# Kernel optimization log

Measured on AMD Instinct MI355X. Metric: run time of the kernel, lower is better.

The kernel has to match this reference:

```python
import jax, jax.numpy as jnp
import numpy as np
import math

DIM, DIM_QK, DIM_V = 1024, 128, 1024
NUM_BUCKETS, MAX_DISTANCE = 32, 128


def silu(x):
    return x * jax.nn.sigmoid(x)


def laplacian_attn_fn(x):
    mu = math.sqrt(0.5)
    std = math.sqrt(0.25 * math.pi)
    return (1.0 + jax.lax.erf((x - mu) / (std * math.sqrt(2.0)))) * 0.5


def rel_pos_bias(seq_len, table, scale):
    # causal T5 bucketing: n = q_pos - k_pos, clamped at 0
    q_pos = jnp.arange(seq_len)
    k_pos = jnp.arange(seq_len)
    rel_pos = k_pos[None, :] - q_pos[:, None]  # [i, j]
    n = jnp.maximum(-rel_pos, 0)
    max_exact = NUM_BUCKETS // 2
    is_small = n < max_exact
    n_safe = jnp.maximum(n, 1).astype(jnp.float32)
    val_if_large = max_exact + (
        jnp.log(n_safe / max_exact) / math.log(MAX_DISTANCE / max_exact)
        * (NUM_BUCKETS - max_exact)
    ).astype(jnp.int32)
    val_if_large = jnp.minimum(val_if_large, NUM_BUCKETS - 1)
    bucket = jnp.where(is_small, n, val_if_large)
    return table[bucket] * scale  # [i, j]


def setup_inputs() -> dict:
    key = jax.random.key(0)
    ks = jax.random.split(key, 8)
    B, S = 4, 2048
    lin_std_qk = 1.0 / math.sqrt(DIM)
    return {
        "x": jax.random.normal(ks[0], (B, S, DIM), dtype=jnp.float32),
        "wqk": jax.random.uniform(ks[1], (DIM, DIM_QK), minval=-lin_std_qk, maxval=lin_std_qk, dtype=jnp.float32),
        "bqk": jnp.zeros((DIM_QK,), dtype=jnp.float32),
        "gamma": 1.0 + 0.02 * jax.random.normal(ks[2], (2, DIM_QK), dtype=jnp.float32),
        "beta": jnp.zeros((2, DIM_QK), dtype=jnp.float32),
        "wv": jax.random.uniform(ks[3], (DIM, DIM_V), minval=-lin_std_qk, maxval=lin_std_qk, dtype=jnp.float32),
        "bv": jnp.zeros((DIM_V,), dtype=jnp.float32),
        "rel_bias": jax.random.normal(ks[4], (NUM_BUCKETS,), dtype=jnp.float32),
    }


def reference(x, wqk, bqk, gamma, beta, wv, bv, rel_bias):
    B, S, _ = x.shape
    qk = silu(x @ wqk + bqk)                       # [B, S, dqk]
    q = qk * gamma[0] + beta[0]
    k = qk * gamma[1] + beta[1]
    v = silu(x @ wv + bv)                          # [B, S, dv]
    scale = 1.0 / S                                # laplacian_attn_fn scaling
    sim = jnp.einsum('bid,bjd->bij', q, k) * scale
    sim = sim + rel_pos_bias(S, rel_bias, DIM_QK ** 0.5)[None, :, :]
    attn = laplacian_attn_fn(sim)
    causal_mask = jnp.triu(jnp.ones((S, S), dtype=bool), k=1)
    attn = jnp.where(causal_mask[None, :, :], 0.0, attn)
    return jnp.einsum('bij,bjd->bid', attn, v)
```

## Files before the change

### kernel.cpp

```cpp
#include <hip/hip_runtime.h>
#include <stdint.h>


#define B_   4
#define S_   2048
#define DIM_ 1024
#define DQK  128
#define DV   1024
#define NQV  1152

typedef __attribute__((ext_vector_type(8))) short short8;
typedef __attribute__((ext_vector_type(4))) float f32x4;

__device__ __forceinline__ uint16_t f32_to_bf16(float f) {
  uint32_t u = __float_as_uint(f);
  u += 0x7FFFu + ((u >> 16) & 1u);
  return (uint16_t)(u >> 16);
}

__device__ __forceinline__ uint32_t pack_bf16(float a, float b) {
  return (uint32_t)f32_to_bf16(a) | ((uint32_t)f32_to_bf16(b) << 16);
}

__device__ __forceinline__ float silu_f(float x) {
  return x * __builtin_amdgcn_rcpf(1.0f + __expf(-x));
}

__device__ __forceinline__ float laplacian_attn(float x) {
  float z  = (x - 0.70710678118654752f) * 0.79788456080286536f;
  float az = fabsf(z);
  float t  = __builtin_amdgcn_rcpf(fmaf(0.3275911f, az, 1.0f));
  float w  = fmaf(1.061405429f, t, -1.453152027f);
  w = fmaf(w, t, 1.421413741f);
  w = fmaf(w, t, -0.284496736f);
  w = fmaf(w, t, 0.254829592f);
  float P  = w * t;
  float E  = __expf(-z * z);
  float ea = fmaf(-P, E, 1.0f);
  float er = copysignf(ea, z);
  return fmaf(0.5f, er, 0.5f);
}

__device__ __forceinline__ void gload16(const uint16_t* g, uint16_t* l) {
  __builtin_amdgcn_global_load_lds(
      (const __attribute__((address_space(1))) void*)g,
      (__attribute__((address_space(3))) void*)l, 16, 0, 0);
}

template <int MT, int NT, int DEPTH>
__device__ __forceinline__ void wave_gemm_t(
    const uint16_t* __restrict__ A, int KBa, int rbA,
    const uint16_t* __restrict__ Bt, int KBb, int rbB,
    int nkb, f32x4 acc[MT][NT])
{
  const int lane = threadIdx.x & 63;

  const uint16_t* pa[MT];
  const uint16_t* pb[NT];
  #pragma unroll
  for (int mt = 0; mt < MT; mt++)
    pa[mt] = A + (size_t)(rbA + mt) * KBa * 512 + lane * 8;
  #pragma unroll
  for (int nt = 0; nt < NT; nt++)
    pb[nt] = Bt + (size_t)(rbB + nt) * KBb * 512 + lane * 8;

  #pragma unroll
  for (int mt = 0; mt < MT; mt++)
    #pragma unroll
    for (int nt = 0; nt < NT; nt++) {
      f32x4 z = {0.0f, 0.0f, 0.0f, 0.0f};
      acc[mt][nt] = z;
    }

  short8 fa0[MT], fb0[NT], fa1[MT], fb1[NT];

  auto loads = [&](short8 fa[MT], short8 fb[NT], int kb) {
    #pragma unroll
    for (int mt = 0; mt < MT; mt++)
      fa[mt] = *(const short8*)(pa[mt] + (size_t)kb * 512);
    #pragma unroll
    for (int nt = 0; nt < NT; nt++)
      fb[nt] = *(const short8*)(pb[nt] + (size_t)kb * 512);
  };
  auto mfmas = [&](short8 fa[MT], short8 fb[NT]) {
    #pragma unroll
    for (int mt = 0; mt < MT; mt++)
      #pragma unroll
      for (int nt = 0; nt < NT; nt++)
        acc[mt][nt] = __builtin_amdgcn_mfma_f32_16x16x32_bf16(
            fa[mt], fb[nt], acc[mt][nt], 0, 0, 0);
  };

  loads(fa0, fb0, 0);
  loads(fa1, fb1, 1);
  for (int kb = 2; kb < nkb; kb += 2) {
    mfmas(fa0, fb0);
    loads(fa0, fb0, kb);
    mfmas(fa1, fb1);
    loads(fa1, fb1, kb + 1);
  }
  mfmas(fa0, fb0);
  mfmas(fa1, fb1);
}

#define WAVE_PREAMBLE                                  \
  int lane = threadIdx.x & 63;                         \
  int wave = threadIdx.x >> 6;                         \
  int lane16 = lane & 15;                              \
  int quad = lane >> 4;                                \
  int wrow = (wave >> 1) * 64;                         \
  int wcol = (wave & 1) * 64;

__global__ __launch_bounds__(256) void k_prep(
    const float* __restrict__ x, const float* __restrict__ wqk,
    const float* __restrict__ wv, const float* __restrict__ rel,
    uint16_t* __restrict__ xb, uint16_t* __restrict__ wT,
    float* __restrict__ bias_n)
{
  int blk = blockIdx.x;
  if (blk < 4096) {
    int t = blk * 256 + threadIdx.x;
    int i16 = t & 15, oct = (t >> 4) & 3, kb = (t >> 6) & 31, ib = t >> 11;
    const float* src = x + (size_t)(ib * 16 + i16) * DIM_ + kb * 32 + oct * 8;
    float4 a = *(const float4*)src;
    float4 b = *(const float4*)(src + 4);
    short8 o;
    o[0] = f32_to_bf16(a.x); o[1] = f32_to_bf16(a.y);
    o[2] = f32_to_bf16(a.z); o[3] = f32_to_bf16(a.w);
    o[4] = f32_to_bf16(b.x); o[5] = f32_to_bf16(b.y);
    o[6] = f32_to_bf16(b.z); o[7] = f32_to_bf16(b.w);
    *(short8*)(xb + (size_t)t * 8) = o;
  } else if (blk < 4672) {
    int t = (blk - 4096) * 256 + threadIdx.x;
    int n16 = t & 15, oct = (t >> 4) & 3, kb = (t >> 6) & 31, nb = t >> 11;
    int n = nb * 16 + n16;
    int k0 = kb * 32 + oct * 8;
    short8 o;
    if (n < DQK) {
      #pragma unroll
      for (int j = 0; j < 8; j++)
        o[j] = f32_to_bf16(wqk[(size_t)(k0 + j) * DQK + n]);
    } else {
      int nn = n - DQK;
      #pragma unroll
      for (int j = 0; j < 8; j++)
        o[j] = f32_to_bf16(wv[(size_t)(k0 + j) * DV + nn]);
    }
    *(short8*)(wT + (size_t)t * 8) = o;
  } else {
    for (int n = threadIdx.x; n < S_; n += 256) {
      int bucket;
      if (n < 16) {
        bucket = n;
      } else {
        float tt = logf((float)n * 0.0625f) / 2.0794415416798357f * 16.0f;
        int vl = 16 + (int)tt;
        bucket = vl < 31 ? vl : 31;
      }
      bias_n[n] = rel[bucket] * 11.313708498984761f;
    }
  }
}


__global__ __launch_bounds__(256, 3) void k_gemm_qkv(
    const uint16_t* __restrict__ xb, const uint16_t* __restrict__ wT,
    const float* __restrict__ bqk, const float* __restrict__ gamma,
    const float* __restrict__ beta, const float* __restrict__ bv,
    uint16_t* __restrict__ qb, uint16_t* __restrict__ kb,
    uint16_t* __restrict__ vT)
{
  int L = blockIdx.x;
  int c = L & 7;
  int idx = L >> 3;
  int by = c + 8 * (idx / 9);
  int bx = idx % 9;
  WAVE_PREAMBLE

  __shared__ uint16_t sA[8 * 2 * 512];
  __shared__ uint16_t sB[8 * 2 * 512];

  const uint16_t *Ab, *Bb;
  if (bx == 0) { Ab = wT;                              Bb = xb + (size_t)by * 8 * 32 * 512; }
  else         { Ab = xb + (size_t)by * 8 * 32 * 512;  Bb = wT + (size_t)bx * 8 * 32 * 512; }

  const uint16_t* gp = (wave >> 1) ? Bb : Ab;
  uint16_t*       sp = (wave >> 1) ? sB : sA;
  int rb0 = (wave & 1) * 4;

  f32x4 acc[4][4];
  #pragma unroll
  for (int mt = 0; mt < 4; mt++)
    #pragma unroll
    for (int nt = 0; nt < 4; nt++) {
      f32x4 z = {0.0f, 0.0f, 0.0f, 0.0f};
      acc[mt][nt] = z;
    }

  for (int kbi = 0; kbi < 32; kbi += 2) {
    #pragma unroll
    for (int uu = 0; uu < 8; uu++) {
      int rbu = rb0 + (uu >> 1), kk = uu & 1;
      gload16(gp + ((size_t)rbu * 32 + kbi + kk) * 512 + lane * 8,
              sp + (rbu * 2 + kk) * 512);
    }
    __syncthreads();
    #pragma unroll
    for (int kk = 0; kk < 2; kk++) {
      short8 fa[4], fb[4];
      #pragma unroll
      for (int mt = 0; mt < 4; mt++)
        fa[mt] = *(const short8*)(sA + (((wave >> 1) * 4 + mt) * 2 + kk) * 512 + lane * 8);
      #pragma unroll
      for (int nt = 0; nt < 4; nt++)
        fb[nt] = *(const short8*)(sB + (((wave & 1) * 4 + nt) * 2 + kk) * 512 + lane * 8);
      #pragma unroll
      for (int mt = 0; mt < 4; mt++)
        #pragma unroll
        for (int nt = 0; nt < 4; nt++)
          acc[mt][nt] = __builtin_amdgcn_mfma_f32_16x16x32_bf16(
              fa[mt], fb[nt], acc[mt][nt], 0, 0, 0);
    }
    __syncthreads();
  }

  if (bx == 0) {
    int ibase = by * 128 + (wave & 1) * 64;
    int cbase = (wave >> 1) * 64;
    #pragma unroll
    for (int mt = 0; mt < 4; mt++) {
      int c0 = cbase + mt * 16 + quad * 4;
      float4 bb = *(const float4*)(bqk + c0);
      float4 g0 = *(const float4*)(gamma + c0);
      float4 g1 = *(const float4*)(gamma + DQK + c0);
      float4 e0 = *(const float4*)(beta + c0);
      float4 e1 = *(const float4*)(beta + DQK + c0);
      size_t coff = (size_t)(c0 >> 5) * 512 + ((c0 >> 3) & 3) * 128 + (c0 & 7);
      #pragma unroll
      for (int nt = 0; nt < 4; nt++) {
        int i = ibase + nt * 16 + lane16;
        float s0 = silu_f(acc[mt][nt][0] + bb.x);
        float s1 = silu_f(acc[mt][nt][1] + bb.y);
        float s2 = silu_f(acc[mt][nt][2] + bb.z);
        float s3 = silu_f(acc[mt][nt][3] + bb.w);
        uint2 pq, pk;
        pq.x = pack_bf16(fmaf(s0, g0.x, e0.x), fmaf(s1, g0.y, e0.y));
        pq.y = pack_bf16(fmaf(s2, g0.z, e0.z), fmaf(s3, g0.w, e0.w));
        pk.x = pack_bf16(fmaf(s0, g1.x, e1.x), fmaf(s1, g1.y, e1.y));
        pk.y = pack_bf16(fmaf(s2, g1.z, e1.z), fmaf(s3, g1.w, e1.w));
        size_t off = (size_t)(i >> 4) * 4 * 512 + (size_t)(i & 15) * 8 + coff;
        *(uint2*)(qb + off) = pq;
        *(uint2*)(kb + off) = pk;
      }
    }
  } else {
    int b = by >> 4;
    uint16_t* vt = vT + (size_t)b * DV * S_;
    #pragma unroll
    for (int nt = 0; nt < 4; nt++) {
      int n = (bx - 1) * 128 + wcol + nt * 16 + lane16;
      float bb = bv[n];
      #pragma unroll
      for (int mt = 0; mt < 4; mt++) {
        int j0l = (by & 15) * 128 + wrow + mt * 16 + quad * 4;
        uint16_t v0 = f32_to_bf16(silu_f(acc[mt][nt][0] + bb));
        uint16_t v1 = f32_to_bf16(silu_f(acc[mt][nt][1] + bb));
        uint16_t v2 = f32_to_bf16(silu_f(acc[mt][nt][2] + bb));
        uint16_t v3 = f32_to_bf16(silu_f(acc[mt][nt][3] + bb));
        size_t off = (size_t)((n >> 4) * 64 + (j0l >> 5)) * 512 +
                     ((j0l >> 3) & 3) * 128 + (n & 15) * 8 + (j0l & 7);
        uint2 pk;
        pk.x = (uint32_t)v0 | ((uint32_t)v1 << 16);
        pk.y = (uint32_t)v2 | ((uint32_t)v3 << 16);
        *(uint2*)(vt + off) = pk;
      }
    }
  }
}

__global__ __launch_bounds__(128, 4) void k_gemm_sim(
    const uint16_t* __restrict__ qb, const uint16_t* __restrict__ kb,
    const float* __restrict__ bias_n, uint16_t* __restrict__ attn)
{
  int b = blockIdx.x;
  int bt = blockIdx.y;
  int it = (int)((sqrtf(8.0f * (float)b + 1.0f) - 1.0f) * 0.5f);
  while ((it + 1) * (it + 2) / 2 <= b) ++it;
  while (it * (it + 1) / 2 > b) --it;
  int jt = b - it * (it + 1) / 2;

  int lane = threadIdx.x & 63;
  int wave = threadIdx.x >> 6;
  int lane16 = lane & 15;
  int quad = lane >> 4;

  f32x4 acc[4][2];
  wave_gemm_t<4,2,2>(kb, 4, bt * 128 + jt * 4,
                     qb, 4, bt * 128 + it * 4 + wave * 2,
                     4, acc);

  uint16_t* ab = attn + (size_t)bt * S_ * S_;
  int ibase = it * 64 + wave * 32;
  int jbase = jt * 64;
  #pragma unroll
  for (int nt = 0; nt < 2; nt++) {
    int i = ibase + nt * 16 + lane16;
    size_t irow = (size_t)(i >> 4) * 64 * 512 + (size_t)(i & 15) * 8;
    #pragma unroll
    for (int mt = 0; mt < 4; mt++) {
      int j0 = jbase + mt * 16 + quad * 4;
      float v[4];
      #pragma unroll
      for (int r = 0; r < 4; r++) {
        int j = j0 + r;
        float aval = 0.0f;
        if (j <= i) {
          float sim = acc[mt][nt][r] * (1.0f / 2048.0f) + bias_n[i - j];
          aval = laplacian_attn(sim);
        }
        v[r] = aval;
      }
      uint2 pk;
      pk.x = pack_bf16(v[0], v[1]);
      pk.y = pack_bf16(v[2], v[3]);
      size_t off = irow + (size_t)(j0 >> 5) * 512 + ((j0 >> 3) & 3) * 128 +
                   (j0 & 7);
      *(uint2*)(ab + off) = pk;
    }
  }
}

__global__ __launch_bounds__(256, 3) void k_gemm_out(
    const uint16_t* __restrict__ attn, const uint16_t* __restrict__ vT,
    float* __restrict__ out)
{
  int L = blockIdx.x;
  int c = L & 7, m = L >> 3;
  int bt = c >> 1;
  int nx = (c & 1) * 4 + (m & 3);
  int it = 15 - (m >> 2);
  int nkb = 4 * it + 4;
  WAVE_PREAMBLE

  __shared__ uint16_t sA[8 * 2 * 512];
  __shared__ uint16_t sB[8 * 2 * 512];

  const uint16_t* Ab = vT + (size_t)bt * DV * S_ + (size_t)nx * 8 * 64 * 512;
  const uint16_t* Bb = attn + (size_t)bt * S_ * S_ + (size_t)it * 8 * 64 * 512;

  const uint16_t* gp = (wave >> 1) ? Bb : Ab;
  uint16_t*       sp = (wave >> 1) ? sB : sA;
  int rb0 = (wave & 1) * 4;

  f32x4 acc[4][4];
  #pragma unroll
  for (int mt = 0; mt < 4; mt++)
    #pragma unroll
    for (int nt = 0; nt < 4; nt++) {
      f32x4 z = {0.0f, 0.0f, 0.0f, 0.0f};
      acc[mt][nt] = z;
    }

  for (int kbi = 0; kbi < nkb; kbi += 2) {
    #pragma unroll
    for (int uu = 0; uu < 8; uu++) {
      int rbu = rb0 + (uu >> 1), kk = uu & 1;
      gload16(gp + ((size_t)rbu * 64 + kbi + kk) * 512 + lane * 8,
              sp + (rbu * 2 + kk) * 512);
    }
    __syncthreads();
    #pragma unroll
    for (int kk = 0; kk < 2; kk++) {
      short8 fa[4], fb[4];
      #pragma unroll
      for (int mt = 0; mt < 4; mt++)
        fa[mt] = *(const short8*)(sA + (((wave & 1) * 4 + mt) * 2 + kk) * 512 + lane * 8);
      #pragma unroll
      for (int nt = 0; nt < 4; nt++)
        fb[nt] = *(const short8*)(sB + (((wave >> 1) * 4 + nt) * 2 + kk) * 512 + lane * 8);
      #pragma unroll
      for (int mt = 0; mt < 4; mt++)
        #pragma unroll
        for (int nt = 0; nt < 4; nt++)
          acc[mt][nt] = __builtin_amdgcn_mfma_f32_16x16x32_bf16(
              fa[mt], fb[nt], acc[mt][nt], 0, 0, 0);
    }
    __syncthreads();
  }

  float* ob = out + ((size_t)bt * S_ + it * 128 + wrow) * DV + nx * 128 + wcol;
  #pragma unroll
  for (int nt = 0; nt < 4; nt++) {
    int i = nt * 16 + lane16;
    #pragma unroll
    for (int mt = 0; mt < 4; mt++) {
      int n = mt * 16 + quad * 4;
      *(float4*)(ob + (size_t)i * DV + n) = *(float4*)&acc[mt][nt];
    }
  }
}


extern "C" void kernel_launch(void* const* d_in, const int* in_sizes, int n_in,
                              void* d_out, int out_size, void* d_ws, size_t ws_size,
                              hipStream_t stream)
{
  const float* x     = (const float*)d_in[0];
  const float* wqk   = (const float*)d_in[1];
  const float* bqk   = (const float*)d_in[2];
  const float* gamma = (const float*)d_in[3];
  const float* beta  = (const float*)d_in[4];
  const float* wv    = (const float*)d_in[5];
  const float* bv    = (const float*)d_in[6];
  const float* rel   = (const float*)d_in[7];
  float* out = (float*)d_out;

  char* ws = (char*)d_ws;
  size_t off = 0;
  uint16_t* xb     = (uint16_t*)(ws + off); off += (size_t)B_ * S_ * DIM_ * 2;
  uint16_t* wT     = (uint16_t*)(ws + off); off += (size_t)NQV * DIM_ * 2;
  uint16_t* qb     = (uint16_t*)(ws + off); off += (size_t)B_ * S_ * DQK * 2;
  uint16_t* kb     = (uint16_t*)(ws + off); off += (size_t)B_ * S_ * DQK * 2;
  uint16_t* vT     = (uint16_t*)(ws + off); off += (size_t)B_ * DV * S_ * 2;
  uint16_t* attn   = (uint16_t*)(ws + off); off += (size_t)B_ * S_ * S_ * 2;
  float*    bias_n = (float*)(ws + off);    off += (size_t)S_ * 4;

  k_prep<<<dim3(4673), dim3(256), 0, stream>>>(x, wqk, wv, rel, xb, wT, bias_n);

  k_gemm_qkv<<<dim3(576), dim3(256), 0, stream>>>(
      xb, wT, bqk, gamma, beta, bv, qb, kb, vT);
  k_gemm_sim<<<dim3(528, B_), dim3(128), 0, stream>>>(
      qb, kb, bias_n, attn);
  k_gemm_out<<<dim3(512), dim3(256), 0, stream>>>(
      attn, vT, out);
}
```

Baseline: 171.0 us.

## Fuse sim and output GEMMs into one kernel with per-row-tile readiness flags

Merges the attention-score kernel and the attn@V kernel into a single launch. Producer blocks compute causal sim tiles, write bf16 attention, then release-increment a per-(batch,row-tile) counter. Consumer blocks spin on that counter before running the output GEMM. The goal is to overlap the two phases and remove the kernel boundary and tail idle time. The wave-level GEMM also gets a deeper 4-stage register prefetch. The spin-wait relies on producer blocks being scheduled ahead of consumers, which adds deadlock risk and adds polling overhead.

```diff
diff --git a/kernel.cpp b/kernel.cpp
--- a/kernel.cpp
+++ b/kernel.cpp
@@ -91,16 +91,38 @@
             fa[mt], fb[nt], acc[mt][nt], 0, 0, 0);
   };
 
-  loads(fa0, fb0, 0);
-  loads(fa1, fb1, 1);
-  for (int kb = 2; kb < nkb; kb += 2) {
+  if constexpr (DEPTH == 2) {
+    loads(fa0, fb0, 0);
+    loads(fa1, fb1, 1);
+    for (int kb = 2; kb < nkb; kb += 2) {
+      mfmas(fa0, fb0);
+      loads(fa0, fb0, kb);
+      mfmas(fa1, fb1);
+      loads(fa1, fb1, kb + 1);
+    }
     mfmas(fa0, fb0);
-    loads(fa0, fb0, kb);
     mfmas(fa1, fb1);
-    loads(fa1, fb1, kb + 1);
+  } else {
+    short8 fa2[MT], fb2[NT], fa3[MT], fb3[NT];
+    loads(fa0, fb0, 0);
+    loads(fa1, fb1, 1);
+    loads(fa2, fb2, 2);
+    loads(fa3, fb3, 3);
+    for (int kb = 4; kb < nkb; kb += 4) {
+      mfmas(fa0, fb0);
+      loads(fa0, fb0, kb);
+      mfmas(fa1, fb1);
+      loads(fa1, fb1, kb + 1);
+      mfmas(fa2, fb2);
+      loads(fa2, fb2, kb + 2);
+      mfmas(fa3, fb3);
+      loads(fa3, fb3, kb + 3);
+    }
+    mfmas(fa0, fb0);
+    mfmas(fa1, fb1);
+    mfmas(fa2, fb2);
+    mfmas(fa3, fb3);
   }
-  mfmas(fa0, fb0);
-  mfmas(fa1, fb1);
 }
 
 #define WAVE_PREAMBLE                                  \
@@ -115,7 +137,7 @@
     const float* __restrict__ x, const float* __restrict__ wqk,
     const float* __restrict__ wv, const float* __restrict__ rel,
     uint16_t* __restrict__ xb, uint16_t* __restrict__ wT,
-    float* __restrict__ bias_n)
+    float* __restrict__ bias_n, uint32_t* __restrict__ flags)
 {
   int blk = blockIdx.x;
   if (blk < 4096) {
@@ -159,9 +181,9 @@
       }
       bias_n[n] = rel[bucket] * 11.313708498984761f;
     }
+    if (threadIdx.x < 64) flags[threadIdx.x] = 0u;
   }
 }
-
 
 __global__ __launch_bounds__(256, 3) void k_gemm_qkv(
     const uint16_t* __restrict__ xb, const uint16_t* __restrict__ wT,
@@ -278,124 +300,153 @@
   }
 }
 
-__global__ __launch_bounds__(128, 4) void k_gemm_sim(
+__global__ __launch_bounds__(256, 3) void k_simout(
     const uint16_t* __restrict__ qb, const uint16_t* __restrict__ kb,
-    const float* __restrict__ bias_n, uint16_t* __restrict__ attn)
+    const float* __restrict__ bias_n, uint16_t* attn,
+    const uint16_t* __restrict__ vT, float* __restrict__ out,
+    uint32_t* flags)
 {
-  int b = blockIdx.x;
-  int bt = blockIdx.y;
-  int it = (int)((sqrtf(8.0f * (float)b + 1.0f) - 1.0f) * 0.5f);
-  while ((it + 1) * (it + 2) / 2 <= b) ++it;
-  while (it * (it + 1) / 2 > b) --it;
-  int jt = b - it * (it + 1) / 2;
+  int Lb = blockIdx.x;
+  int c = Lb & 7, r = Lb >> 3;
+  int H = 15 - c;
+
+  __shared__ uint16_t sA[8 * 2 * 512];
+  __shared__ uint16_t sB[8 * 2 * 512];
 
   int lane = threadIdx.x & 63;
   int wave = threadIdx.x >> 6;
   int lane16 = lane & 15;
   int quad = lane >> 4;
 
-  f32x4 acc[4][2];
-  wave_gemm_t<4,2,2>(kb, 4, bt * 128 + jt * 4,
-                     qb, 4, bt * 128 + it * 4 + wave * 2,
-                     4, acc);
-
-  uint16_t* ab = attn + (size_t)bt * S_ * S_;
-  int ibase = it * 64 + wave * 32;
-  int jbase = jt * 64;
-  #pragma unroll
-  for (int nt = 0; nt < 2; nt++) {
-    int i = ibase + nt * 16 + lane16;
-    size_t irow = (size_t)(i >> 4) * 64 * 512 + (size_t)(i & 15) * 8;
-    #pragma unroll
-    for (int mt = 0; mt < 4; mt++) {
-      int j0 = jbase + mt * 16 + quad * 4;
-      float v[4];
-      #pragma unroll
-      for (int r = 0; r < 4; r++) {
-        int j = j0 + r;
-        float aval = 0.0f;
-        if (j <= i) {
-          float sim = acc[mt][nt][r] * (1.0f / 2048.0f) + bias_n[i - j];
-          aval = laplacian_attn(sim);
+  if (r < 132) {
+    int t = 2 * r + (wave >> 1);
+    int bt, it64, jt;
+    {
+      int nHt = 4 * H + 3, baseH = 4 * nHt;
+      if (t < baseH) {
+        bt = t / nHt;
+        int u = t - bt * nHt;
+        if (u <= 2 * H) { it64 = 2 * H; jt = u; }
+        else            { it64 = 2 * H + 1; jt = u - (2 * H + 1); }
+      } else {
+        int nLt = 4 * c + 3;
+        int t2 = t - baseH;
+        bt = t2 / nLt;
+        int u = t2 - bt * nLt;
+        if (u <= 2 * c) { it64 = 2 * c; jt = u; }
+        else            { it64 = 2 * c + 1; jt = u - (2 * c + 1); }
+      }
+    }
+    int wv = wave & 1;
+
+    f32x4 acc[4][2];
+    wave_gemm_t<4,2,4>(kb, 4, bt * 128 + jt * 4,
+                       qb, 4, bt * 128 + it64 * 4 + wv * 2,
+                       4, acc);
+
+    uint16_t* ab = attn + (size_t)bt * S_ * S_;
+    int ibase = it64 * 64 + wv * 32;
+    int jbase = jt * 64;
+    #pragma unroll
+    for (int nt = 0; nt < 2; nt++) {
+      int i = ibase + nt * 16 + lane16;
+      size_t irow = (size_t)(i >> 4) * 64 * 512 + (size_t)(i & 15) * 8;
+      #pragma unroll
+      for (int mt = 0; mt < 4; mt++) {
+        int j0 = jbase + mt * 16 + quad * 4;
+        float v[4];
+        #pragma unroll
+        for (int rr = 0; rr < 4; rr++) {
+          int j = j0 + rr;
+          float aval = 0.0f;
+          if (j <= i) {
+            float sim = acc[mt][nt][rr] * (1.0f / 2048.0f) + bias_n[i - j];
+            aval = laplacian_attn(sim);
+          }
+          v[rr] = aval;
         }
-        v[r] = aval;
-      }
-      uint2 pk;
-      pk.x = pack_bf16(v[0], v[1]);
-      pk.y = pack_bf16(v[2], v[3]);
-      size_t off = irow + (size_t)(j0 >> 5) * 512 + ((j0 >> 3) & 3) * 128 +
-                   (j0 & 7);
-      *(uint2*)(ab + off) = pk;
-    }
-  }
-}
-
-__global__ __launch_bounds__(256, 3) void k_gemm_out(
-    const uint16_t* __restrict__ attn, const uint16_t* __restrict__ vT,
-    float* __restrict__ out)
-{
-  int L = blockIdx.x;
-  int c = L & 7, m = L >> 3;
-  int bt = c >> 1;
-  int nx = (c & 1) * 4 + (m & 3);
-  int it = 15 - (m >> 2);
-  int nkb = 4 * it + 4;
-  WAVE_PREAMBLE
-
-  __shared__ uint16_t sA[8 * 2 * 512];
-  __shared__ uint16_t sB[8 * 2 * 512];
-
-  const uint16_t* Ab = vT + (size_t)bt * DV * S_ + (size_t)nx * 8 * 64 * 512;
-  const uint16_t* Bb = attn + (size_t)bt * S_ * S_ + (size_t)it * 8 * 64 * 512;
-
-  const uint16_t* gp = (wave >> 1) ? Bb : Ab;
-  uint16_t*       sp = (wave >> 1) ? sB : sA;
-  int rb0 = (wave & 1) * 4;
-
-  f32x4 acc[4][4];
-  #pragma unroll
-  for (int mt = 0; mt < 4; mt++)
-    #pragma unroll
-    for (int nt = 0; nt < 4; nt++) {
-      f32x4 z = {0.0f, 0.0f, 0.0f, 0.0f};
-      acc[mt][nt] = z;
-    }
-
-  for (int kbi = 0; kbi < nkb; kbi += 2) {
-    #pragma unroll
-    for (int uu = 0; uu < 8; uu++) {
-      int rbu = rb0 + (uu >> 1), kk = uu & 1;
-      gload16(gp + ((size_t)rbu * 64 + kbi + kk) * 512 + lane * 8,
-              sp + (rbu * 2 + kk) * 512);
-    }
+        uint2 pk;
+        pk.x = pack_bf16(v[0], v[1]);
+        pk.y = pack_bf16(v[2], v[3]);
+        size_t off = irow + (size_t)(j0 >> 5) * 512 + ((j0 >> 3) & 3) * 128 +
+                     (j0 & 7);
+        *(uint2*)(ab + off) = pk;
+      }
+    }
+
+    __threadfence();
     __syncthreads();
-    #pragma unroll
-    for (int kk = 0; kk < 2; kk++) {
-      short8 fa[4], fb[4];
-      #pragma unroll
-      for (int mt = 0; mt < 4; mt++)
-        fa[mt] = *(const short8*)(sA + (((wave & 1) * 4 + mt) * 2 + kk) * 512 + lane * 8);
-      #pragma unroll
-      for (int nt = 0; nt < 4; nt++)
-        fb[nt] = *(const short8*)(sB + (((wave >> 1) * 4 + nt) * 2 + kk) * 512 + lane * 8);
-      #pragma unroll
-      for (int mt = 0; mt < 4; mt++)
+    if ((threadIdx.x & 127) == 0)
+      __hip_atomic_fetch_add(&flags[bt * 16 + (it64 >> 1)], 1u,
+                             __ATOMIC_RELEASE, __HIP_MEMORY_SCOPE_AGENT);
+  } else {
+    int o = r - 132;
+    int it = (o < 32) ? H : c;
+    int bt = (o >> 3) & 3, nx = o & 7;
+    int nkb = 4 * it + 4;
+
+    if (threadIdx.x == 0) {
+      while (__hip_atomic_load(&flags[bt * 16 + it], __ATOMIC_ACQUIRE,
+                               __HIP_MEMORY_SCOPE_AGENT) < (uint32_t)(4 * it + 3))
+        __builtin_amdgcn_s_sleep(2);
+    }
+    __syncthreads();
+
+    int wrow = (wave >> 1) * 64;
+    int wcol = (wave & 1) * 64;
+
+    const uint16_t* Ab = vT + (size_t)bt * DV * S_ + (size_t)nx * 8 * 64 * 512;
+    const uint16_t* Bb = attn + (size_t)bt * S_ * S_ + (size_t)it * 8 * 64 * 512;
+
+    const uint16_t* gp = (wave >> 1) ? Bb : Ab;
+    uint16_t*       sp = (wave >> 1) ? sB : sA;
+    int rb0 = (wave & 1) * 4;
+
+    f32x4 acc[4][4];
+    #pragma unroll
+    for (int mt = 0; mt < 4; mt++)
+      #pragma unroll
+      for (int nt = 0; nt < 4; nt++) {
+        f32x4 z = {0.0f, 0.0f, 0.0f, 0.0f};
+        acc[mt][nt] = z;
+      }
+
+    for (int kbi = 0; kbi < nkb; kbi += 2) {
+      #pragma unroll
+      for (int uu = 0; uu < 8; uu++) {
+        int rbu = rb0 + (uu >> 1), kk = uu & 1;
+        gload16(gp + ((size_t)rbu * 64 + kbi + kk) * 512 + lane * 8,
+                sp + (rbu * 2 + kk) * 512);
+      }
+      __syncthreads();
+      #pragma unroll
+      for (int kk = 0; kk < 2; kk++) {
+        short8 fa[4], fb[4];
+        #pragma unroll
+        for (int mt = 0; mt < 4; mt++)
+          fa[mt] = *(const short8*)(sA + (((wave & 1) * 4 + mt) * 2 + kk) * 512 + lane * 8);
         #pragma unroll
         for (int nt = 0; nt < 4; nt++)
-          acc[mt][nt] = __builtin_amdgcn_mfma_f32_16x16x32_bf16(
-              fa[mt], fb[nt], acc[mt][nt], 0, 0, 0);
-    }
-    __syncthreads();
-  }
-
-  float* ob = out + ((size_t)bt * S_ + it * 128 + wrow) * DV + nx * 128 + wcol;
-  #pragma unroll
-  for (int nt = 0; nt < 4; nt++) {
-    int i = nt * 16 + lane16;
-    #pragma unroll
-    for (int mt = 0; mt < 4; mt++) {
-      int n = mt * 16 + quad * 4;
-      *(float4*)(ob + (size_t)i * DV + n) = *(float4*)&acc[mt][nt];
+          fb[nt] = *(const short8*)(sB + (((wave >> 1) * 4 + nt) * 2 + kk) * 512 + lane * 8);
+        #pragma unroll
+        for (int mt = 0; mt < 4; mt++)
+          #pragma unroll
+          for (int nt = 0; nt < 4; nt++)
+            acc[mt][nt] = __builtin_amdgcn_mfma_f32_16x16x32_bf16(
+                fa[mt], fb[nt], acc[mt][nt], 0, 0, 0);
+      }
+      __syncthreads();
+    }
+
+    float* ob = out + ((size_t)bt * S_ + it * 128 + wrow) * DV + nx * 128 + wcol;
+    #pragma unroll
+    for (int nt = 0; nt < 4; nt++) {
+      int i = nt * 16 + lane16;
+      #pragma unroll
+      for (int mt = 0; mt < 4; mt++) {
+        int n = mt * 16 + quad * 4;
+        *(float4*)(ob + (size_t)i * DV + n) = *(float4*)&acc[mt][nt];
+      }
     }
   }
 }
@@ -424,13 +475,12 @@
   uint16_t* vT     = (uint16_t*)(ws + off); off += (size_t)B_ * DV * S_ * 2;
   uint16_t* attn   = (uint16_t*)(ws + off); off += (size_t)B_ * S_ * S_ * 2;
   float*    bias_n = (float*)(ws + off);    off += (size_t)S_ * 4;
-
-  k_prep<<<dim3(4673), dim3(256), 0, stream>>>(x, wqk, wv, rel, xb, wT, bias_n);
-
+  uint32_t* flags  = (uint32_t*)(ws + off); off += 64 * 4;
+
+  k_prep<<<dim3(4673), dim3(256), 0, stream>>>(x, wqk, wv, rel, xb, wT,
+                                               bias_n, flags);
   k_gemm_qkv<<<dim3(576), dim3(256), 0, stream>>>(
       xb, wT, bqk, gamma, beta, bv, qb, kb, vT);
-  k_gemm_sim<<<dim3(528, B_), dim3(128), 0, stream>>>(
-      qb, kb, bias_n, attn);
-  k_gemm_out<<<dim3(512), dim3(256), 0, stream>>>(
-      attn, vT, out);
-}
+  k_simout<<<dim3(1568), dim3(256), 0, stream>>>(
+      qb, kb, bias_n, attn, vT, out, flags);
+}
```

Measured after the change: 399.2 us. 133% more time.

## Split QK projection out and co-schedule V projection with similarity kernel

Applied to the files above, without the earlier changes.

The QKV projection kernel is split. A small 64-block kernel now computes only Q/K. The V projection blocks are merged into the similarity kernel's grid, so the sim tiles (two per 256-thread block) run concurrently with the V GEMM tiles in one launch. The wave-level GEMM helper also gains a depth-4 register prefetch variant, used by the sim path. The goal is better GPU fill by overlapping the sim work, which depends only on Q/K, with the large V GEMM. The cost is a tiny, poorly occupied QK kernel serialized in front, plus heavier register pressure from the deeper prefetch.

```diff
diff --git a/kernel.cpp b/kernel.cpp
--- a/kernel.cpp
+++ b/kernel.cpp
@@ -91,25 +91,39 @@
             fa[mt], fb[nt], acc[mt][nt], 0, 0, 0);
   };
 
-  loads(fa0, fb0, 0);
-  loads(fa1, fb1, 1);
-  for (int kb = 2; kb < nkb; kb += 2) {
+  if constexpr (DEPTH == 2) {
+    loads(fa0, fb0, 0);
+    loads(fa1, fb1, 1);
+    for (int kb = 2; kb < nkb; kb += 2) {
+      mfmas(fa0, fb0);
+      loads(fa0, fb0, kb);
+      mfmas(fa1, fb1);
+      loads(fa1, fb1, kb + 1);
+    }
     mfmas(fa0, fb0);
-    loads(fa0, fb0, kb);
     mfmas(fa1, fb1);
-    loads(fa1, fb1, kb + 1);
-  }
-  mfmas(fa0, fb0);
-  mfmas(fa1, fb1);
-}
-
-#define WAVE_PREAMBLE                                  \
-  int lane = threadIdx.x & 63;                         \
-  int wave = threadIdx.x >> 6;                         \
-  int lane16 = lane & 15;                              \
-  int quad = lane >> 4;                                \
-  int wrow = (wave >> 1) * 64;                         \
-  int wcol = (wave & 1) * 64;
+  } else {
+    short8 fa2[MT], fb2[NT], fa3[MT], fb3[NT];
+    loads(fa0, fb0, 0);
+    loads(fa1, fb1, 1);
+    loads(fa2, fb2, 2);
+    loads(fa3, fb3, 3);
+    for (int kb = 4; kb < nkb; kb += 4) {
+      mfmas(fa0, fb0);
+      loads(fa0, fb0, kb);
+      mfmas(fa1, fb1);
+      loads(fa1, fb1, kb + 1);
+      mfmas(fa2, fb2);
+      loads(fa2, fb2, kb + 2);
+      mfmas(fa3, fb3);
+      loads(fa3, fb3, kb + 3);
+    }
+    mfmas(fa0, fb0);
+    mfmas(fa1, fb1);
+    mfmas(fa2, fb2);
+    mfmas(fa3, fb3);
+  }
+}
 
 __global__ __launch_bounds__(256) void k_prep(
     const float* __restrict__ x, const float* __restrict__ wqk,
@@ -162,27 +176,24 @@
   }
 }
 
-
-__global__ __launch_bounds__(256, 3) void k_gemm_qkv(
+__global__ __launch_bounds__(256, 3) void k_gemm_qk(
     const uint16_t* __restrict__ xb, const uint16_t* __restrict__ wT,
     const float* __restrict__ bqk, const float* __restrict__ gamma,
-    const float* __restrict__ beta, const float* __restrict__ bv,
-    uint16_t* __restrict__ qb, uint16_t* __restrict__ kb,
-    uint16_t* __restrict__ vT)
+    const float* __restrict__ beta,
+    uint16_t* __restrict__ qb, uint16_t* __restrict__ kb)
 {
   int L = blockIdx.x;
-  int c = L & 7;
-  int idx = L >> 3;
-  int by = c + 8 * (idx / 9);
-  int bx = idx % 9;
-  WAVE_PREAMBLE
+  int by = (L & 7) + 8 * (L >> 3);
+  int lane = threadIdx.x & 63;
+  int wave = threadIdx.x >> 6;
+  int lane16 = lane & 15;
+  int quad = lane >> 4;
 
   __shared__ uint16_t sA[8 * 2 * 512];
   __shared__ uint16_t sB[8 * 2 * 512];
 
-  const uint16_t *Ab, *Bb;
-  if (bx == 0) { Ab = wT;                              Bb = xb + (size_t)by * 8 * 32 * 512; }
-  else         { Ab = xb + (size_t)by * 8 * 32 * 512;  Bb = wT + (size_t)bx * 8 * 32 * 512; }
+  const uint16_t* Ab = wT;
+  const uint16_t* Bb = xb + (size_t)by * 8 * 32 * 512;
 
   const uint16_t* gp = (wave >> 1) ? Bb : Ab;
   uint16_t*       sp = (wave >> 1) ? sB : sA;
@@ -224,36 +235,146 @@
     __syncthreads();
   }
 
-  if (bx == 0) {
-    int ibase = by * 128 + (wave & 1) * 64;
-    int cbase = (wave >> 1) * 64;
-    #pragma unroll
-    for (int mt = 0; mt < 4; mt++) {
-      int c0 = cbase + mt * 16 + quad * 4;
-      float4 bb = *(const float4*)(bqk + c0);
-      float4 g0 = *(const float4*)(gamma + c0);
-      float4 g1 = *(const float4*)(gamma + DQK + c0);
-      float4 e0 = *(const float4*)(beta + c0);
-      float4 e1 = *(const float4*)(beta + DQK + c0);
-      size_t coff = (size_t)(c0 >> 5) * 512 + ((c0 >> 3) & 3) * 128 + (c0 & 7);
+  int ibase = by * 128 + (wave & 1) * 64;
+  int cbase = (wave >> 1) * 64;
+  #pragma unroll
+  for (int mt = 0; mt < 4; mt++) {
+    int c0 = cbase + mt * 16 + quad * 4;
+    float4 bb = *(const float4*)(bqk + c0);
+    float4 g0 = *(const float4*)(gamma + c0);
+    float4 g1 = *(const float4*)(gamma + DQK + c0);
+    float4 e0 = *(const float4*)(beta + c0);
+    float4 e1 = *(const float4*)(beta + DQK + c0);
+    size_t coff = (size_t)(c0 >> 5) * 512 + ((c0 >> 3) & 3) * 128 + (c0 & 7);
+    #pragma unroll
+    for (int nt = 0; nt < 4; nt++) {
+      int i = ibase + nt * 16 + lane16;
+      float s0 = silu_f(acc[mt][nt][0] + bb.x);
+      float s1 = silu_f(acc[mt][nt][1] + bb.y);
+      float s2 = silu_f(acc[mt][nt][2] + bb.z);
+      float s3 = silu_f(acc[mt][nt][3] + bb.w);
+      uint2 pq, pk;
+      pq.x = pack_bf16(fmaf(s0, g0.x, e0.x), fmaf(s1, g0.y, e0.y));
+      pq.y = pack_bf16(fmaf(s2, g0.z, e0.z), fmaf(s3, g0.w, e0.w));
+      pk.x = pack_bf16(fmaf(s0, g1.x, e1.x), fmaf(s1, g1.y, e1.y));
+      pk.y = pack_bf16(fmaf(s2, g1.z, e1.z), fmaf(s3, g1.w, e1.w));
+      size_t off = (size_t)(i >> 4) * 4 * 512 + (size_t)(i & 15) * 8 + coff;
+      *(uint2*)(qb + off) = pq;
+      *(uint2*)(kb + off) = pk;
+    }
+  }
+}
+
+__global__ __launch_bounds__(256, 4) void k_simv(
+    const uint16_t* __restrict__ qb, const uint16_t* __restrict__ kb,
+    const float* __restrict__ bias_n, uint16_t* __restrict__ attn,
+    const uint16_t* __restrict__ xb, const uint16_t* __restrict__ wT,
+    const float* __restrict__ bv, uint16_t* __restrict__ vT)
+{
+  int Lb = blockIdx.x;
+  int lane = threadIdx.x & 63;
+  int wave = threadIdx.x >> 6;
+  int lane16 = lane & 15;
+  int quad = lane >> 4;
+
+  __shared__ uint16_t sA[8 * 2 * 512];
+  __shared__ uint16_t sB[8 * 2 * 512];
+
+  if (Lb < 1056) {
+    int t = 2 * Lb + (wave >> 1);
+    int bt = t / 528;
+    int u = t - bt * 528;
+    int it = (int)((sqrtf(8.0f * (float)u + 1.0f) - 1.0f) * 0.5f);
+    while ((it + 1) * (it + 2) / 2 <= u) ++it;
+    while (it * (it + 1) / 2 > u) --it;
+    int jt = u - it * (it + 1) / 2;
+    int wv = wave & 1;
+
+    f32x4 acc[4][2];
+    wave_gemm_t<4,2,4>(kb, 4, bt * 128 + jt * 4,
+                       qb, 4, bt * 128 + it * 4 + wv * 2,
+                       4, acc);
+
+    uint16_t* ab = attn + (size_t)bt * S_ * S_;
+    int ibase = it * 64 + wv * 32;
+    int jbase = jt * 64;
+    #pragma unroll
+    for (int nt = 0; nt < 2; nt++) {
+      int i = ibase + nt * 16 + lane16;
+      size_t irow = (size_t)(i >> 4) * 64 * 512 + (size_t)(i & 15) * 8;
+      #pragma unroll
+      for (int mt = 0; mt < 4; mt++) {
+        int j0 = jbase + mt * 16 + quad * 4;
+        float v[4];
+        #pragma unroll
+        for (int rr = 0; rr < 4; rr++) {
+          int j = j0 + rr;
+          float aval = 0.0f;
+          if (j <= i) {
+            float sim = acc[mt][nt][rr] * (1.0f / 2048.0f) + bias_n[i - j];
+            aval = laplacian_attn(sim);
+          }
+          v[rr] = aval;
+        }
+        uint2 pk;
+        pk.x = pack_bf16(v[0], v[1]);
+        pk.y = pack_bf16(v[2], v[3]);
+        size_t off = irow + (size_t)(j0 >> 5) * 512 + ((j0 >> 3) & 3) * 128 +
+                     (j0 & 7);
+        *(uint2*)(ab + off) = pk;
+      }
+    }
+  } else {
+    int o = Lb - 1056;
+    int c = o & 7;
+    int by = c + 8 * ((o >> 3) & 7);
+    int bx = 1 + (o >> 6);
+    int wrow = (wave >> 1) * 64;
+    int wcol = (wave & 1) * 64;
+
+    const uint16_t* Ab = xb + (size_t)by * 8 * 32 * 512;
+    const uint16_t* Bb = wT + (size_t)bx * 8 * 32 * 512;
+
+    const uint16_t* gp = (wave >> 1) ? Bb : Ab;
+    uint16_t*       sp = (wave >> 1) ? sB : sA;
+    int rb0 = (wave & 1) * 4;
+
+    f32x4 acc[4][4];
+    #pragma unroll
+    for (int mt = 0; mt < 4; mt++)
       #pragma unroll
       for (int nt = 0; nt < 4; nt++) {
-        int i = ibase + nt * 16 + lane16;
-        float s0 = silu_f(acc[mt][nt][0] + bb.x);
-        float s1 = silu_f(acc[mt][nt][1] + bb.y);
-        float s2 = silu_f(acc[mt][nt][2] + bb.z);
-        float s3 = silu_f(acc[mt][nt][3] + bb.w);
-        uint2 pq, pk;
-        pq.x = pack_bf16(fmaf(s0, g0.x, e0.x), fmaf(s1, g0.y, e0.y));
-        pq.y = pack_bf16(fmaf(s2, g0.z, e0.z), fmaf(s3, g0.w, e0.w));
-        pk.x = pack_bf16(fmaf(s0, g1.x, e1.x), fmaf(s1, g1.y, e1.y));
-        pk.y = pack_bf16(fmaf(s2, g1.z, e1.z), fmaf(s3, g1.w, e1.w));
-        size_t off = (size_t)(i >> 4) * 4 * 512 + (size_t)(i & 15) * 8 + coff;
-        *(uint2*)(qb + off) = pq;
-        *(uint2*)(kb + off) = pk;
+        f32x4 z = {0.0f, 0.0f, 0.0f, 0.0f};
+        acc[mt][nt] = z;
       }
-    }
-  } else {
+
+    for (int kbi = 0; kbi < 32; kbi += 2) {
+      #pragma unroll
+      for (int uu = 0; uu < 8; uu++) {
+        int rbu = rb0 + (uu >> 1), kk = uu & 1;
+        gload16(gp + ((size_t)rbu * 32 + kbi + kk) * 512 + lane * 8,
+                sp + (rbu * 2 + kk) * 512);
+      }
+      __syncthreads();
+      #pragma unroll
+      for (int kk = 0; kk < 2; kk++) {
+        short8 fa[4], fb[4];
+        #pragma unroll
+        for (int mt = 0; mt < 4; mt++)
+          fa[mt] = *(const short8*)(sA + (((wave >> 1) * 4 + mt) * 2 + kk) * 512 + lane * 8);
+        #pragma unroll
+        for (int nt = 0; nt < 4; nt++)
+          fb[nt] = *(const short8*)(sB + (((wave & 1) * 4 + nt) * 2 + kk) * 512 + lane * 8);
+        #pragma unroll
+        for (int mt = 0; mt < 4; mt++)
+          #pragma unroll
+          for (int nt = 0; nt < 4; nt++)
+            acc[mt][nt] = __builtin_amdgcn_mfma_f32_16x16x32_bf16(
+                fa[mt], fb[nt], acc[mt][nt], 0, 0, 0);
+      }
+      __syncthreads();
+    }
+
     int b = by >> 4;
     uint16_t* vt = vT + (size_t)b * DV * S_;
     #pragma unroll
@@ -278,58 +399,6 @@
   }
 }
 
-__global__ __launch_bounds__(128, 4) void k_gemm_sim(
-    const uint16_t* __restrict__ qb, const uint16_t* __restrict__ kb,
-    const float* __restrict__ bias_n, uint16_t* __restrict__ attn)
-{
-  int b = blockIdx.x;
-  int bt = blockIdx.y;
-  int it = (int)((sqrtf(8.0f * (float)b + 1.0f) - 1.0f) * 0.5f);
-  while ((it + 1) * (it + 2) / 2 <= b) ++it;
-  while (it * (it + 1) / 2 > b) --it;
-  int jt = b - it * (it + 1) / 2;
-
-  int lane = threadIdx.x & 63;
-  int wave = threadIdx.x >> 6;
-  int lane16 = lane & 15;
-  int quad = lane >> 4;
-
-  f32x4 acc[4][2];
-  wave_gemm_t<4,2,2>(kb, 4, bt * 128 + jt * 4,
-                     qb, 4, bt * 128 + it * 4 + wave * 2,
-                     4, acc);
-
-  uint16_t* ab = attn + (size_t)bt * S_ * S_;
-  int ibase = it * 64 + wave * 32;
-  int jbase = jt * 64;
-  #pragma unroll
-  for (int nt = 0; nt < 2; nt++) {
-    int i = ibase + nt * 16 + lane16;
-    size_t irow = (size_t)(i >> 4) * 64 * 512 + (size_t)(i & 15) * 8;
-    #pragma unroll
-    for (int mt = 0; mt < 4; mt++) {
-      int j0 = jbase + mt * 16 + quad * 4;
-      float v[4];
-      #pragma unroll
-      for (int r = 0; r < 4; r++) {
-        int j = j0 + r;
-        float aval = 0.0f;
-        if (j <= i) {
-          float sim = acc[mt][nt][r] * (1.0f / 2048.0f) + bias_n[i - j];
-          aval = laplacian_attn(sim);
-        }
-        v[r] = aval;
-      }
-      uint2 pk;
-      pk.x = pack_bf16(v[0], v[1]);
-      pk.y = pack_bf16(v[2], v[3]);
-      size_t off = irow + (size_t)(j0 >> 5) * 512 + ((j0 >> 3) & 3) * 128 +
-                   (j0 & 7);
-      *(uint2*)(ab + off) = pk;
-    }
-  }
-}
-
 __global__ __launch_bounds__(256, 3) void k_gemm_out(
     const uint16_t* __restrict__ attn, const uint16_t* __restrict__ vT,
     float* __restrict__ out)
@@ -340,7 +409,12 @@
   int nx = (c & 1) * 4 + (m & 3);
   int it = 15 - (m >> 2);
   int nkb = 4 * it + 4;
-  WAVE_PREAMBLE
+  int lane = threadIdx.x & 63;
+  int wave = threadIdx.x >> 6;
+  int lane16 = lane & 15;
+  int quad = lane >> 4;
+  int wrow = (wave >> 1) * 64;
+  int wcol = (wave & 1) * 64;
 
   __shared__ uint16_t sA[8 * 2 * 512];
   __shared__ uint16_t sB[8 * 2 * 512];
@@ -426,11 +500,10 @@
   float*    bias_n = (float*)(ws + off);    off += (size_t)S_ * 4;
 
   k_prep<<<dim3(4673), dim3(256), 0, stream>>>(x, wqk, wv, rel, xb, wT, bias_n);
-
-  k_gemm_qkv<<<dim3(576), dim3(256), 0, stream>>>(
-      xb, wT, bqk, gamma, beta, bv, qb, kb, vT);
-  k_gemm_sim<<<dim3(528, B_), dim3(128), 0, stream>>>(
-      qb, kb, bias_n, attn);
+  k_gemm_qk<<<dim3(64), dim3(256), 0, stream>>>(
+      xb, wT, bqk, gamma, beta, qb, kb);
+  k_simv<<<dim3(1568), dim3(256), 0, stream>>>(
+      qb, kb, bias_n, attn, xb, wT, bv, vT);
   k_gemm_out<<<dim3(512), dim3(256), 0, stream>>>(
       attn, vT, out);
 }
```

After: 183.5 us. 1.07x slower.
